# Kernel optimization log

Measured on AMD Instinct MI355X. Metric: run time of the kernel, lower is better.

## Reference

```python
import jax, jax.numpy as jnp
import numpy as np

N_NODE = 50000
N_EDGE = 625000
FDIM = 128
HID = 128
EPS = 1e-5


def setup_inputs() -> dict:
    key = jax.random.key(0)
    ks = jax.random.split(key, 12)
    node_feature = jax.random.normal(ks[0], (N_NODE, FDIM), dtype=jnp.float32)
    edge_matrix = jax.random.randint(ks[1], (2, N_EDGE), 0, N_NODE, dtype=jnp.int32)
    edge_feature = jax.random.normal(ks[2], (N_EDGE, FDIM), dtype=jnp.float32)
    in_dim = FDIM + FDIM  # concat(node, aggregated edge)
    s1 = 1.0 / np.sqrt(in_dim)
    s2 = 1.0 / np.sqrt(HID)
    W1 = jax.random.uniform(ks[3], (in_dim, HID), jnp.float32, -s1, s1)
    b1 = jax.random.uniform(ks[4], (HID,), jnp.float32, -s1, s1)
    W2 = jax.random.uniform(ks[5], (HID, HID), jnp.float32, -s2, s2)
    b2 = jax.random.uniform(ks[6], (HID,), jnp.float32, -s2, s2)
    W3 = jax.random.uniform(ks[7], (HID, FDIM), jnp.float32, -s2, s2)
    b3 = jax.random.uniform(ks[8], (FDIM,), jnp.float32, -s2, s2)
    gamma = jnp.ones((FDIM,), jnp.float32)
    beta = jnp.zeros((FDIM,), jnp.float32)
    return {"node_feature": node_feature, "edge_matrix": edge_matrix,
            "edge_feature": edge_feature, "W1": W1, "b1": b1, "W2": W2,
            "b2": b2, "W3": W3, "b3": b3, "gamma": gamma, "beta": beta}


def reference(node_feature, edge_matrix, edge_feature, W1, b1, W2, b2, W3, b3, gamma, beta):
    # receiver_idx = edge_matrix.T[:, 1] with edge_matrix [2, N_edge] -> row 1
    receiver_idx = edge_matrix[1]
    # scatter_add over receiver: [N_node, fdim]
    agg = jax.ops.segment_sum(edge_feature, receiver_idx, num_segments=node_feature.shape[0])
    x = jnp.concatenate([node_feature, agg], axis=-1)  # [N_node, 2*fdim]
    h = jax.nn.relu(x @ W1 + b1)
    h = jax.nn.relu(h @ W2 + b2)
    h = h @ W3 + b3
    # LayerNorm over last dim (eps = 1e-5, torch default)
    mu = jnp.mean(h, axis=-1, keepdims=True)
    var = jnp.mean((h - mu) ** 2, axis=-1, keepdims=True)
    h = (h - mu) * jax.lax.rsqrt(var + EPS) * gamma + beta
    return h + node_feature
```

## Files before the change

kernel.cpp:

```cpp
#include <hip/hip_runtime.h>
#include <hip/hip_bf16.h>

#define N_NODE 50000
#define N_EDGE 625000
#define FDIM 128
#define CAP 64

typedef __bf16 bf16x8 __attribute__((ext_vector_type(8)));
typedef float floatx4 __attribute__((ext_vector_type(4)));

#define MT 32
#define XS_LD 264
#define H_LD 136

__device__ inline bf16x8 as_bf16x8(uint4 v) {
    union { uint4 u; bf16x8 b; } c; c.u = v; return c.b;
}

__global__ __launch_bounds__(256) void wrepack_kernel(
    const float* __restrict__ W1, const float* __restrict__ W2,
    const float* __restrict__ W3, uint4* __restrict__ wp,
    int* __restrict__ count)
{
    if (blockIdx.x >= 32) {
        int idx = (blockIdx.x - 32) * 256 + threadIdx.x;
        for (int i = idx; i < N_NODE; i += 32 * 256) count[i] = 0;
        return;
    }
    int g = blockIdx.x * 256 + threadIdx.x;
    int lane = g & 63;
    int nt = (g >> 6) & 7;
    int tile = g >> 9;
    const float* W; int k0;
    if (tile < 8)       { W = W1; k0 = tile * 32; }
    else if (tile < 12) { W = W2; k0 = (tile - 8) * 32; }
    else                { W = W3; k0 = (tile - 12) * 32; }
    int n = nt * 16 + (lane & 15);
    int kb = k0 + (lane >> 4) * 8;
    union { __bf16 b[8]; uint4 u; } p;
#pragma unroll
    for (int j = 0; j < 8; ++j) p.b[j] = (__bf16)W[(kb + j) * 128 + n];
    wp[g] = p.u;
}

__global__ __launch_bounds__(256) void scatter_kernel(
    const int4* __restrict__ recv4, int* __restrict__ count, int* __restrict__ eid)
{
    int tid = blockIdx.x * 256 + threadIdx.x;
    if (tid < N_EDGE / 4) {
        int4 r = recv4[tid];
        int e0 = tid * 4;
        int p0 = atomicAdd(&count[r.x], 1);
        int p1 = atomicAdd(&count[r.y], 1);
        int p2 = atomicAdd(&count[r.z], 1);
        int p3 = atomicAdd(&count[r.w], 1);
        if (p0 < CAP) eid[(r.x << 6) + p0] = e0;
        if (p1 < CAP) eid[(r.y << 6) + p1] = e0 + 1;
        if (p2 < CAP) eid[(r.z << 6) + p2] = e0 + 2;
        if (p3 < CAP) eid[(r.w << 6) + p3] = e0 + 3;
    }
}

__global__ __launch_bounds__(256) void gather_kernel(
    const float4* __restrict__ ef4, const int* __restrict__ count,
    const int* __restrict__ eid, uint2* __restrict__ agg)
{
    int wave = threadIdx.x >> 6;
    int lane = threadIdx.x & 63;
    int node = blockIdx.x * 4 + wave;
    int half = lane >> 5;
    int c = lane & 31;
    float4 acc = {0.f, 0.f, 0.f, 0.f};
    int ids = eid[(node << 6) + lane];
    int cnt = count[node]; if (cnt > CAP) cnt = CAP;
    int j = 0;
    for (; j + 8 <= cnt; j += 8) {
        int ea = __shfl(ids, j + half);
        int eb = __shfl(ids, j + 2 + half);
        int ec = __shfl(ids, j + 4 + half);
        int ed = __shfl(ids, j + 6 + half);
        float4 va = ef4[(long)ea * 32 + c];
        float4 vb = ef4[(long)eb * 32 + c];
        float4 vc = ef4[(long)ec * 32 + c];
        float4 vd = ef4[(long)ed * 32 + c];
        acc.x += va.x + vb.x + vc.x + vd.x;
        acc.y += va.y + vb.y + vc.y + vd.y;
        acc.z += va.z + vb.z + vc.z + vd.z;
        acc.w += va.w + vb.w + vc.w + vd.w;
    }
    if (j + 4 <= cnt) {
        int ea = __shfl(ids, j + half);
        int eb = __shfl(ids, j + 2 + half);
        float4 va = ef4[(long)ea * 32 + c];
        float4 vb = ef4[(long)eb * 32 + c];
        acc.x += va.x + vb.x; acc.y += va.y + vb.y;
        acc.z += va.z + vb.z; acc.w += va.w + vb.w;
        j += 4;
    }
    if (j + 2 <= cnt) {
        int e = __shfl(ids, j + half);
        float4 v = ef4[(long)e * 32 + c];
        acc.x += v.x; acc.y += v.y; acc.z += v.z; acc.w += v.w;
        j += 2;
    }
    if (j + half < cnt) {
        int e = __shfl(ids, j + half);
        float4 v = ef4[(long)e * 32 + c];
        acc.x += v.x; acc.y += v.y; acc.z += v.z; acc.w += v.w;
    }
    acc.x += __shfl_xor(acc.x, 32);
    acc.y += __shfl_xor(acc.y, 32);
    acc.z += __shfl_xor(acc.z, 32);
    acc.w += __shfl_xor(acc.w, 32);
    if (half == 0) {
        union { __bf16 b[4]; uint2 u; } p;
        p.b[0] = (__bf16)acc.x; p.b[1] = (__bf16)acc.y;
        p.b[2] = (__bf16)acc.z; p.b[3] = (__bf16)acc.w;
        agg[(long)node * 32 + c] = p.u;
    }
}

__global__ __launch_bounds__(256, 5) void mlp_kernel(
    const float* __restrict__ nodef, const int* __restrict__ agg32,
    const uint4* __restrict__ wp,
    const float* __restrict__ b1, const float* __restrict__ b2,
    const float* __restrict__ b3,
    const float* __restrict__ gamma, const float* __restrict__ beta,
    float* __restrict__ out)
{
    __shared__ __bf16 smem[8704];
    __shared__ float red[2][32][2];
    __bf16* xs = smem;
    __bf16* h1 = smem;
    __bf16* h2 = smem + 4352;

    const int t = threadIdx.x;
    const int wave = t >> 6;
    const int lane = t & 63;
    const int quad = lane >> 4;
    const int l16 = lane & 15;
    const int tile = wave >> 1;
    const int ch   = wave & 1;
    const int trow = tile << 4;
    const int q8 = quad << 3;
    const int node0 = blockIdx.x * MT;

    const float4* nf4 = (const float4*)nodef;
#pragma unroll
    for (int i = 0; i < 4; ++i) {
        int it = i * 256 + t;
        int row = it >> 5;
        int c4 = it & 31;
        int node = node0 + row;
        if (node >= N_NODE) node = N_NODE - 1;
        float4 v = nf4[(long)node * 32 + c4];
        union { __bf16 b[4]; short4 s; } u;
        u.b[0] = (__bf16)v.x; u.b[1] = (__bf16)v.y;
        u.b[2] = (__bf16)v.z; u.b[3] = (__bf16)v.w;
        *(short4*)&xs[row * XS_LD + c4 * 4] = u.s;
    }
    const int4* ag4 = (const int4*)agg32;
#pragma unroll
    for (int i = 0; i < 2; ++i) {
        int it = i * 256 + t;
        int row = it >> 4;
        int c8 = it & 15;
        int node = node0 + row;
        if (node >= N_NODE) node = N_NODE - 1;
        int4 v = ag4[(long)node * 16 + c8];
        *(int4*)&xs[row * XS_LD + 128 + c8 * 8] = v;
    }

    floatx4 acc[4];
    const floatx4 zero = {0.f, 0.f, 0.f, 0.f};

    auto run_gemm = [&](const __bf16* A, int ldA, const uint4* __restrict__ wpt, int nk) {
#pragma unroll
        for (int nt = 0; nt < 4; ++nt) acc[nt] = zero;
        const __bf16* arow = A + (trow + l16) * ldA + q8;
        const uint4* wc = wpt + (ch << 2) * 64;
        bf16x8 a = *(const bf16x8*)arow;
        bf16x8 bA[4], bB[4];
#pragma unroll
        for (int i = 0; i < 4; ++i) bA[i] = as_bf16x8(wc[i * 64 + lane]);
        for (int kc = 0; kc < nk; ++kc) {
            bf16x8 a2 = a;
            if (kc + 1 < nk) {
                const uint4* wn = wc + (kc + 1) * 512;
#pragma unroll
                for (int i = 0; i < 4; ++i) bB[i] = as_bf16x8(wn[i * 64 + lane]);
                a2 = *(const bf16x8*)(arow + (kc + 1) * 32);
            }
#pragma unroll
            for (int nt = 0; nt < 4; ++nt)
                acc[nt] = __builtin_amdgcn_mfma_f32_16x16x32_bf16(a, bA[nt], acc[nt], 0, 0, 0);
            a = a2;
#pragma unroll
            for (int i = 0; i < 4; ++i) bA[i] = bB[i];
        }
    };

    auto epilogue_relu = [&](const float* __restrict__ bias, __bf16* H) {
#pragma unroll
        for (int nt = 0; nt < 4; ++nt) {
            int col = (ch << 6) + nt * 16 + l16;
            float bv = bias[col];
#pragma unroll
            for (int r = 0; r < 4; ++r) {
                float v = acc[nt][r] + bv;
                v = v > 0.f ? v : 0.f;
                H[(trow + quad * 4 + r) * H_LD + col] = (__bf16)v;
            }
        }
    };

    __syncthreads();
    run_gemm(xs, XS_LD, wp, 8);
    __syncthreads();
    epilogue_relu(b1, h1);
    __syncthreads();
    run_gemm(h1, H_LD, wp + 4096, 4);
    epilogue_relu(b2, h2);
    __syncthreads();
    run_gemm(h2, H_LD, wp + 6144, 4);

    float vout[4][4];
    float sum[4] = {0.f, 0.f, 0.f, 0.f};
    float sq[4]  = {0.f, 0.f, 0.f, 0.f};
#pragma unroll
    for (int nt = 0; nt < 4; ++nt) {
        int col = (ch << 6) + nt * 16 + l16;
        float bv = b3[col];
#pragma unroll
        for (int r = 0; r < 4; ++r) {
            float v = acc[nt][r] + bv;
            vout[nt][r] = v;
            sum[r] += v;
            sq[r] += v * v;
        }
    }
#pragma unroll
    for (int r = 0; r < 4; ++r) {
#pragma unroll
        for (int offs = 1; offs < 16; offs <<= 1) {
            sum[r] += __shfl_xor(sum[r], offs);
            sq[r]  += __shfl_xor(sq[r], offs);
        }
    }
    if (l16 == 0) {
#pragma unroll
        for (int r = 0; r < 4; ++r) {
            red[ch][trow + quad * 4 + r][0] = sum[r];
            red[ch][trow + quad * 4 + r][1] = sq[r];
        }
    }
    __syncthreads();
    float mu[4], rs[4];
#pragma unroll
    for (int r = 0; r < 4; ++r) {
        int row = trow + quad * 4 + r;
        float s = red[0][row][0] + red[1][row][0];
        float q = red[0][row][1] + red[1][row][1];
        mu[r] = s * (1.f / 128.f);
        float var = q * (1.f / 128.f) - mu[r] * mu[r];
        rs[r] = rsqrtf(var + 1e-5f);
    }
#pragma unroll
    for (int nt = 0; nt < 4; ++nt) {
        int col = (ch << 6) + nt * 16 + l16;
        float g = gamma[col], be = beta[col];
#pragma unroll
        for (int r = 0; r < 4; ++r) {
            int row = trow + quad * 4 + r;
            int node = node0 + row;
            if (node < N_NODE) {
                long o = (long)node * 128 + col;
                out[o] = (vout[nt][r] - mu[r]) * rs[r] * g + be + nodef[o];
            }
        }
    }
}

extern "C" void kernel_launch(void* const* d_in, const int* in_sizes, int n_in,
                              void* d_out, int out_size, void* d_ws, size_t ws_size,
                              hipStream_t stream)
{
    const float* nodef = (const float*)d_in[0];
    const int*   em    = (const int*)d_in[1];
    const float* ef    = (const float*)d_in[2];
    const float* W1    = (const float*)d_in[3];
    const float* b1    = (const float*)d_in[4];
    const float* W2    = (const float*)d_in[5];
    const float* b2    = (const float*)d_in[6];
    const float* W3    = (const float*)d_in[7];
    const float* b3    = (const float*)d_in[8];
    const float* gamma = (const float*)d_in[9];
    const float* beta  = (const float*)d_in[10];
    float* out = (float*)d_out;

    int* count = (int*)d_ws;
    int* agg32 = count + 50048;
    uint4* wp  = (uint4*)(agg32 + 3200000);

    int* eid = (int*)d_out;

    const int* recv = em + N_EDGE;

    wrepack_kernel<<<64, 256, 0, stream>>>(W1, W2, W3, wp, count);

    int sblocks = (N_EDGE / 4 + 255) / 256;
    scatter_kernel<<<sblocks, 256, 0, stream>>>((const int4*)recv, count, eid);
    gather_kernel<<<N_NODE / 4, 256, 0, stream>>>((const float4*)ef, count, eid, (uint2*)agg32);

    int mblocks = (N_NODE + MT - 1) / MT;
    mlp_kernel<<<mblocks, 256, 0, stream>>>(nodef, agg32, wp, b1, b2, b3,
                                            gamma, beta, out);
}
```

Baseline: 529.2 us.

## Merge weight repack, scatter and gather into one cooperative kernel

Replaces three separate launches (weight repack plus count clear, edge scatter, edge gather) with a single cooperative kernel of 1024 blocks that uses grid-wide syncs between the phases. The gather phase becomes a grid-stride loop over node groups. This removes two kernel launches and their inter-kernel gaps, in exchange for grid.sync costs and a fixed grid size that may reduce parallelism in the gather phase.

New measurement: 806.3 us. 1.52x slower.

```diff
diff --git a/kernel.cpp b/kernel.cpp
--- a/kernel.cpp
+++ b/kernel.cpp
@@ -1,5 +1,8 @@
 #include <hip/hip_runtime.h>
 #include <hip/hip_bf16.h>
+#include <hip/hip_cooperative_groups.h>
+
+namespace cg = cooperative_groups;
 
 #define N_NODE 50000
 #define N_EDGE 625000
@@ -13,40 +16,42 @@
 #define XS_LD 264
 #define H_LD 136
 
+#define PREP_BLOCKS 1024
+
 __device__ inline bf16x8 as_bf16x8(uint4 v) {
     union { uint4 u; bf16x8 b; } c; c.u = v; return c.b;
 }
 
-__global__ __launch_bounds__(256) void wrepack_kernel(
+__global__ __launch_bounds__(256) void prep_kernel(
     const float* __restrict__ W1, const float* __restrict__ W2,
     const float* __restrict__ W3, uint4* __restrict__ wp,
-    int* __restrict__ count)
+    int* __restrict__ count, const int4* __restrict__ recv4,
+    int* __restrict__ eid, const float4* __restrict__ ef4,
+    uint2* __restrict__ agg)
 {
-    if (blockIdx.x >= 32) {
-        int idx = (blockIdx.x - 32) * 256 + threadIdx.x;
-        for (int i = idx; i < N_NODE; i += 32 * 256) count[i] = 0;
-        return;
-    }
-    int g = blockIdx.x * 256 + threadIdx.x;
-    int lane = g & 63;
-    int nt = (g >> 6) & 7;
-    int tile = g >> 9;
-    const float* W; int k0;
-    if (tile < 8)       { W = W1; k0 = tile * 32; }
-    else if (tile < 12) { W = W2; k0 = (tile - 8) * 32; }
-    else                { W = W3; k0 = (tile - 12) * 32; }
-    int n = nt * 16 + (lane & 15);
-    int kb = k0 + (lane >> 4) * 8;
-    union { __bf16 b[8]; uint4 u; } p;
-#pragma unroll
-    for (int j = 0; j < 8; ++j) p.b[j] = (__bf16)W[(kb + j) * 128 + n];
-    wp[g] = p.u;
-}
-
-__global__ __launch_bounds__(256) void scatter_kernel(
-    const int4* __restrict__ recv4, int* __restrict__ count, int* __restrict__ eid)
-{
-    int tid = blockIdx.x * 256 + threadIdx.x;
+    cg::grid_group grid = cg::this_grid();
+    const int tid = blockIdx.x * 256 + threadIdx.x;
+
+    if (tid < 8192) {
+        int g = tid;
+        int lane = g & 63;
+        int nt = (g >> 6) & 7;
+        int tile = g >> 9;
+        const float* W; int k0;
+        if (tile < 8)       { W = W1; k0 = tile * 32; }
+        else if (tile < 12) { W = W2; k0 = (tile - 8) * 32; }
+        else                { W = W3; k0 = (tile - 12) * 32; }
+        int n = nt * 16 + (lane & 15);
+        int kb = k0 + (lane >> 4) * 8;
+        union { __bf16 b[8]; uint4 u; } p;
+#pragma unroll
+        for (int j = 0; j < 8; ++j) p.b[j] = (__bf16)W[(kb + j) * 128 + n];
+        wp[g] = p.u;
+    }
+    if (tid < N_NODE) count[tid] = 0;
+
+    grid.sync();
+
     if (tid < N_EDGE / 4) {
         int4 r = recv4[tid];
         int e0 = tid * 4;
@@ -59,64 +64,63 @@
         if (p2 < CAP) eid[(r.z << 6) + p2] = e0 + 2;
         if (p3 < CAP) eid[(r.w << 6) + p3] = e0 + 3;
     }
-}
-
-__global__ __launch_bounds__(256) void gather_kernel(
-    const float4* __restrict__ ef4, const int* __restrict__ count,
-    const int* __restrict__ eid, uint2* __restrict__ agg)
-{
-    int wave = threadIdx.x >> 6;
-    int lane = threadIdx.x & 63;
-    int node = blockIdx.x * 4 + wave;
-    int half = lane >> 5;
-    int c = lane & 31;
-    float4 acc = {0.f, 0.f, 0.f, 0.f};
-    int ids = eid[(node << 6) + lane];
-    int cnt = count[node]; if (cnt > CAP) cnt = CAP;
-    int j = 0;
-    for (; j + 8 <= cnt; j += 8) {
-        int ea = __shfl(ids, j + half);
-        int eb = __shfl(ids, j + 2 + half);
-        int ec = __shfl(ids, j + 4 + half);
-        int ed = __shfl(ids, j + 6 + half);
-        float4 va = ef4[(long)ea * 32 + c];
-        float4 vb = ef4[(long)eb * 32 + c];
-        float4 vc = ef4[(long)ec * 32 + c];
-        float4 vd = ef4[(long)ed * 32 + c];
-        acc.x += va.x + vb.x + vc.x + vd.x;
-        acc.y += va.y + vb.y + vc.y + vd.y;
-        acc.z += va.z + vb.z + vc.z + vd.z;
-        acc.w += va.w + vb.w + vc.w + vd.w;
-    }
-    if (j + 4 <= cnt) {
-        int ea = __shfl(ids, j + half);
-        int eb = __shfl(ids, j + 2 + half);
-        float4 va = ef4[(long)ea * 32 + c];
-        float4 vb = ef4[(long)eb * 32 + c];
-        acc.x += va.x + vb.x; acc.y += va.y + vb.y;
-        acc.z += va.z + vb.z; acc.w += va.w + vb.w;
-        j += 4;
-    }
-    if (j + 2 <= cnt) {
-        int e = __shfl(ids, j + half);
-        float4 v = ef4[(long)e * 32 + c];
-        acc.x += v.x; acc.y += v.y; acc.z += v.z; acc.w += v.w;
-        j += 2;
-    }
-    if (j + half < cnt) {
-        int e = __shfl(ids, j + half);
-        float4 v = ef4[(long)e * 32 + c];
-        acc.x += v.x; acc.y += v.y; acc.z += v.z; acc.w += v.w;
-    }
-    acc.x += __shfl_xor(acc.x, 32);
-    acc.y += __shfl_xor(acc.y, 32);
-    acc.z += __shfl_xor(acc.z, 32);
-    acc.w += __shfl_xor(acc.w, 32);
-    if (half == 0) {
-        union { __bf16 b[4]; uint2 u; } p;
-        p.b[0] = (__bf16)acc.x; p.b[1] = (__bf16)acc.y;
-        p.b[2] = (__bf16)acc.z; p.b[3] = (__bf16)acc.w;
-        agg[(long)node * 32 + c] = p.u;
+    __threadfence();
+    grid.sync();
+
+    const int wave = threadIdx.x >> 6;
+    const int lane = threadIdx.x & 63;
+    const int half = lane >> 5;
+    const int c = lane & 31;
+    for (int g = blockIdx.x; g < N_NODE / 4; g += PREP_BLOCKS) {
+        int node = g * 4 + wave;
+        float4 acc = {0.f, 0.f, 0.f, 0.f};
+        int ids = eid[(node << 6) + lane];
+        int cnt = count[node]; if (cnt > CAP) cnt = CAP;
+        int j = 0;
+        for (; j + 8 <= cnt; j += 8) {
+            int ea = __shfl(ids, j + half);
+            int eb = __shfl(ids, j + 2 + half);
+            int ec = __shfl(ids, j + 4 + half);
+            int ed = __shfl(ids, j + 6 + half);
+            float4 va = ef4[(long)ea * 32 + c];
+            float4 vb = ef4[(long)eb * 32 + c];
+            float4 vc = ef4[(long)ec * 32 + c];
+            float4 vd = ef4[(long)ed * 32 + c];
+            acc.x += va.x + vb.x + vc.x + vd.x;
+            acc.y += va.y + vb.y + vc.y + vd.y;
+            acc.z += va.z + vb.z + vc.z + vd.z;
+            acc.w += va.w + vb.w + vc.w + vd.w;
+        }
+        if (j + 4 <= cnt) {
+            int ea = __shfl(ids, j + half);
+            int eb = __shfl(ids, j + 2 + half);
+            float4 va = ef4[(long)ea * 32 + c];
+            float4 vb = ef4[(long)eb * 32 + c];
+            acc.x += va.x + vb.x; acc.y += va.y + vb.y;
+            acc.z += va.z + vb.z; acc.w += va.w + vb.w;
+            j += 4;
+        }
+        if (j + 2 <= cnt) {
+            int e = __shfl(ids, j + half);
+            float4 v = ef4[(long)e * 32 + c];
+            acc.x += v.x; acc.y += v.y; acc.z += v.z; acc.w += v.w;
+            j += 2;
+        }
+        if (j + half < cnt) {
+            int e = __shfl(ids, j + half);
+            float4 v = ef4[(long)e * 32 + c];
+            acc.x += v.x; acc.y += v.y; acc.z += v.z; acc.w += v.w;
+        }
+        acc.x += __shfl_xor(acc.x, 32);
+        acc.y += __shfl_xor(acc.y, 32);
+        acc.z += __shfl_xor(acc.z, 32);
+        acc.w += __shfl_xor(acc.w, 32);
+        if (half == 0) {
+            union { __bf16 b[4]; uint2 u; } p;
+            p.b[0] = (__bf16)acc.x; p.b[1] = (__bf16)acc.y;
+            p.b[2] = (__bf16)acc.z; p.b[3] = (__bf16)acc.w;
+            agg[(long)node * 32 + c] = p.u;
+        }
     }
 }
 
@@ -305,12 +309,15 @@
     int* eid = (int*)d_out;
 
     const int* recv = em + N_EDGE;
-
-    wrepack_kernel<<<64, 256, 0, stream>>>(W1, W2, W3, wp, count);
-
-    int sblocks = (N_EDGE / 4 + 255) / 256;
-    scatter_kernel<<<sblocks, 256, 0, stream>>>((const int4*)recv, count, eid);
-    gather_kernel<<<N_NODE / 4, 256, 0, stream>>>((const float4*)ef, count, eid, (uint2*)agg32);
+    const int4* recv4 = (const int4*)recv;
+    const float4* ef4 = (const float4*)ef;
+    uint2* agg = (uint2*)agg32;
+
+    void* args[] = { (void*)&W1, (void*)&W2, (void*)&W3, (void*)&wp,
+                     (void*)&count, (void*)&recv4, (void*)&eid,
+                     (void*)&ef4, (void*)&agg };
+    hipLaunchCooperativeKernel((void*)prep_kernel, dim3(PREP_BLOCKS), dim3(256),
+                               args, 0, stream);
 
     int mblocks = (N_NODE + MT - 1) / MT;
     mlp_kernel<<<mblocks, 256, 0, stream>>>(nodef, agg32, wp, b1, b2, b3,
```
